# Performance work log

Hardware: AMD Instinct MI355X
Metric: run time of the kernel (lower is better)

Reference implementation:

```python
import jax, jax.numpy as jnp
import numpy as np

WS = 7        # window_size
SHIFT = 3     # shift_size
NH = 12       # num_heads
HD = 32       # head_dim
C = 384       # dim
HH = 56       # height
WW = 56       # width
EPS = 1e-5


def _rel_pos_index():
    coords = np.stack(np.meshgrid(np.arange(WS), np.arange(WS), indexing='ij')).reshape(2, -1)
    rel = (coords[:, :, None] - coords[:, None, :]).transpose(1, 2, 0)
    rel[:, :, 0] += WS - 1
    rel[:, :, 1] += WS - 1
    rel[:, :, 0] *= 2 * WS - 1
    return rel.sum(-1)  # (49, 49) int


def _attn_mask():
    # shift mask, computed statically (shift_size > 0 path)
    img = np.zeros((HH, WW))
    slices = (slice(0, -WS), slice(-WS, -SHIFT), slice(-SHIFT, None))
    cnt = 0
    for hs in slices:
        for ws in slices:
            img[hs, ws] = cnt
            cnt += 1
    mw = img.reshape(HH // WS, WS, WW // WS, WS).transpose(0, 2, 1, 3).reshape(-1, WS * WS)
    diff = mw[:, None, :] - mw[:, :, None]  # (nW, 49, 49)
    return np.where(diff != 0, -100.0, 0.0).astype(np.float32)


_REL_IDX = jnp.asarray(_rel_pos_index())
_MASK = jnp.asarray(_attn_mask())


def _layernorm(x, g, b):
    mu = jnp.mean(x, axis=-1, keepdims=True)
    var = jnp.mean(jnp.square(x - mu), axis=-1, keepdims=True)
    return (x - mu) * jax.lax.rsqrt(var + EPS) * g + b


def setup_inputs() -> dict:
    key = jax.random.key(0)
    ks = jax.random.split(key, 10)
    s = 0.02
    return {
        'hidden_states': jax.random.normal(ks[0], (32, HH * WW, C), jnp.float32),
        'ln1_g': jnp.ones((C,), jnp.float32),
        'ln1_b': jnp.zeros((C,), jnp.float32),
        'qkv_w': jax.random.normal(ks[1], (3 * C, C), jnp.float32) * s,
        'qkv_b': jnp.zeros((3 * C,), jnp.float32),
        'out_w': jax.random.normal(ks[2], (C, C), jnp.float32) * s,
        'out_b': jnp.zeros((C,), jnp.float32),
        'rel_bias_table': jax.random.normal(ks[3], ((2 * WS - 1) ** 2, NH), jnp.float32) * s,
        'ln2_g': jnp.ones((C,), jnp.float32),
        'ln2_b': jnp.zeros((C,), jnp.float32),
        'fc1_w': jax.random.normal(ks[4], (4 * C, C), jnp.float32) * s,
        'fc1_b': jnp.zeros((4 * C,), jnp.float32),
        'fc2_w': jax.random.normal(ks[5], (C, 4 * C), jnp.float32) * s,
        'fc2_b': jnp.zeros((C,), jnp.float32),
        'height': HH,
        'width': WW,
    }


def reference(hidden_states, ln1_g, ln1_b, qkv_w, qkv_b, out_w, out_b,
              rel_bias_table, ln2_g, ln2_b, fc1_w, fc1_b, fc2_w, fc2_b,
              height, width):
    B = hidden_states.shape[0]
    nWh, nWw = HH // WS, WW // WS
    nW = nWh * nWw
    L = WS * WS

    shortcut = hidden_states
    x = _layernorm(hidden_states, ln1_g, ln1_b).reshape(B, HH, WW, C)
    x = jnp.roll(x, (-SHIFT, -SHIFT), axis=(1, 2))
    # window partition -> (B*nW, 49, C)
    xw = x.reshape(B, nWh, WS, nWw, WS, C).transpose(0, 1, 3, 2, 4, 5).reshape(B * nW, L, C)

    qkv = xw @ qkv_w.T + qkv_b
    q, k, v = jnp.split(qkv, 3, axis=-1)
    q = q.reshape(-1, L, NH, HD).transpose(0, 2, 1, 3)  # (N, h, 49, d)
    k = k.reshape(-1, L, NH, HD).transpose(0, 2, 1, 3)
    v = v.reshape(-1, L, NH, HD).transpose(0, 2, 1, 3)

    scale = HD ** -0.5
    attn = jnp.einsum('nhqd,nhkd->nhqk', q, k) * scale
    bias = rel_bias_table[_REL_IDX.reshape(-1)].reshape(L, L, NH).transpose(2, 0, 1)  # (h, 49, 49)
    attn = attn + bias[None]
    attn = attn.reshape(B, nW, NH, L, L) + _MASK[None, :, None]
    attn = jax.nn.softmax(attn, axis=-1).reshape(B * nW, NH, L, L)

    out = jnp.einsum('nhqk,nhkd->nhqd', attn, v).transpose(0, 2, 1, 3).reshape(B * nW, L, C)
    out = out @ out_w.T + out_b

    # window reverse + un-shift
    out = out.reshape(B, nWh, nWw, WS, WS, C).transpose(0, 1, 3, 2, 4, 5).reshape(B, HH, WW, C)
    out = jnp.roll(out, (SHIFT, SHIFT), axis=(1, 2)).reshape(B, HH * WW, C)

    x = shortcut + out  # drop_path is identity (rate 0 / eval)
    h2 = _layernorm(x, ln2_g, ln2_b)
    mlp = jax.nn.gelu(h2 @ fc1_w.T + fc1_b, approximate=False) @ fc2_w.T + fc2_b
    return x + mlp
```

## Files before the change

### kernel.cpp

```cpp
#include <hip/hip_runtime.h>
#include <cstdint>
#include <cstddef>

using u16 = unsigned short;
using u32 = unsigned int;

typedef __attribute__((ext_vector_type(8))) short bf16x8;
typedef __attribute__((ext_vector_type(4))) float f32x4;

__device__ __forceinline__ u16 f2bf(float f) {
  union { float f; u32 u; } v; v.f = f;
  u32 r = v.u + 0x7FFFu + ((v.u >> 16) & 1u);
  return (u16)(r >> 16);
}
__device__ __forceinline__ float bf2f(u16 h) {
  union { u32 u; float f; } v; v.u = ((u32)h) << 16;
  return v.f;
}

__device__ __forceinline__ void gl_lds16(const void* g, void* l) {
  __builtin_amdgcn_global_load_lds(
      (const __attribute__((address_space(1))) void*)g,
      (__attribute__((address_space(3))) void*)l, 16, 0, 0);
}

__global__ __launch_bounds__(256) void k_f2bf(const float* __restrict__ s,
                                              u16* __restrict__ d, int n) {
  int i = blockIdx.x * 256 + threadIdx.x;
  if (i < n) d[i] = f2bf(s[i]);
}

__global__ __launch_bounds__(256) void k_tbl(const float* __restrict__ relt,
                                             float* __restrict__ tbl) {
  int id = blockIdx.x * 256 + threadIdx.x;
  if (id >= 196608) return;
  int i = id & 63, j = (id >> 6) & 63;
  int wt = (id >> 12) & 3, h = id >> 14;
  float v;
  if (j >= 49) {
    v = -3e38f;
  } else {
    int ii = i < 49 ? i : 48;
    int r1 = ii / 7, c1 = ii % 7, r2 = j / 7, c2 = j % 7;
    v = relt[((r1 - r2 + 6) * 13 + (c1 - c2 + 6)) * 12 + h];
    int rr1 = (wt & 2) ? (r1 < 4 ? 1 : 2) : 0;
    int rr2 = (wt & 2) ? (r2 < 4 ? 1 : 2) : 0;
    int cc1 = (wt & 1) ? (c1 < 4 ? 1 : 2) : 0;
    int cc2 = (wt & 1) ? (c2 < 4 ? 1 : 2) : 0;
    if (rr1 != rr2 || cc1 != cc2) v -= 100.f;
  }
  tbl[id] = v;
}

template <int GATHER>
__global__ __launch_bounds__(256) void k_ln(const float* __restrict__ x,
                                            const float* __restrict__ g,
                                            const float* __restrict__ b,
                                            u16* __restrict__ out) {
  int wave = threadIdx.x >> 6, lane = threadIdx.x & 63;
  int idx = blockIdx.x * 4 + wave;
  int src;
  if (GATHER) {
    int n = idx / 49, l = idx % 49;
    int bb = n >> 6, wi = n & 63;
    int wh = wi >> 3, ww = wi & 7;
    int r = l / 7, c = l % 7;
    int sr = wh * 7 + r + 3; if (sr >= 56) sr -= 56;
    int sc = ww * 7 + c + 3; if (sc >= 56) sc -= 56;
    src = bb * 3136 + sr * 56 + sc;
  } else {
    src = idx;
  }
  const float* xi = x + (size_t)src * 384;
  float2 v[3];
  float s = 0.f, sq = 0.f;
#pragma unroll
  for (int p = 0; p < 3; ++p) {
    v[p] = *(const float2*)(xi + p * 128 + lane * 2);
    s += v[p].x + v[p].y;
    sq += v[p].x * v[p].x + v[p].y * v[p].y;
  }
#pragma unroll
  for (int o = 32; o; o >>= 1) {
    s += __shfl_xor(s, o);
    sq += __shfl_xor(sq, o);
  }
  float mu = s * (1.f / 384.f);
  float var = sq * (1.f / 384.f) - mu * mu;
  float rstd = rsqrtf(var + 1e-5f);
  u16* oo = out + (size_t)idx * 384;
#pragma unroll
  for (int p = 0; p < 3; ++p) {
    int e = p * 128 + lane * 2;
    u16 o0 = f2bf((v[p].x - mu) * rstd * g[e] + b[e]);
    u16 o1 = f2bf((v[p].y - mu) * rstd * g[e + 1] + b[e + 1]);
    u32 pk = (u32)o0 | ((u32)o1 << 16);
    *(u32*)(oo + e) = pk;
  }
}

enum { EPI_QKV = 0, EPI_PROJ = 1, EPI_GELU = 2, EPI_FC2 = 3 };

template <int EPI>
__global__ __launch_bounds__(512, 2) void k_gemm3(
    const u16* __restrict__ A, const u16* __restrict__ Bw,
    const float* __restrict__ bias, u16* __restrict__ obf,
    float* __restrict__ of32, const float* __restrict__ addsrc,
    int K, int lda, int ldb, int ldc, int NT) {
  __shared__ u16 As[256 * 64];
  __shared__ u16 Bs[128 * 64];
  const int nwg = gridDim.x;
  const int q = nwg >> 3, r = nwg & 7;
  const int xcd = blockIdx.x & 7, rank = blockIdx.x >> 3;
  const int swz = (xcd < r ? xcd * (q + 1) : r * (q + 1) + (xcd - r) * q) + rank;
  const int m0 = (swz / NT) * 256, n0 = (swz % NT) * 128;

  const int tid = threadIdx.x;
  const int wid = tid >> 6, lane = tid & 63;
  const int wr = wid >> 1, wc = wid & 1;

  const int srow = tid >> 3;
  const int scol = 8 * ((tid & 7) ^ (srow & 7));
  const size_t abase = (size_t)(m0 + srow) * lda + scol;
  const size_t bbase = (size_t)(n0 + srow) * ldb + scol;
  const int dbase = wid * 512;

  f32x4 acc[4][4] = {};
  const int lrow = lane & 15;
  const int g8 = (lane >> 4) * 8;
  const int rx = (lrow & 7) << 3;

  const int NTK = K >> 6;

  for (int t = 0; t < NTK; ++t) {
    const int k0 = t << 6;
#pragma unroll
    for (int i = 0; i < 4; ++i)
      gl_lds16(A + abase + (size_t)(i * 64) * lda + k0,
               As + i * 4096 + dbase);
#pragma unroll
    for (int i = 0; i < 2; ++i)
      gl_lds16(Bw + bbase + (size_t)(i * 64) * ldb + k0,
               Bs + i * 4096 + dbase);
    __syncthreads();
    __builtin_amdgcn_s_setprio(1);
#pragma unroll
    for (int kk = 0; kk < 64; kk += 32) {
      bf16x8 af[4], bf[4];
#pragma unroll
      for (int mi = 0; mi < 4; ++mi) {
        int row = wr * 64 + mi * 16 + lrow;
        af[mi] = *(const bf16x8*)(&As[row * 64 + ((kk + g8) ^ rx)]);
      }
#pragma unroll
      for (int ni = 0; ni < 4; ++ni) {
        int row = wc * 64 + ni * 16 + lrow;
        bf[ni] = *(const bf16x8*)(&Bs[row * 64 + ((kk + g8) ^ rx)]);
      }
#pragma unroll
      for (int mi = 0; mi < 4; ++mi)
#pragma unroll
        for (int ni = 0; ni < 4; ++ni)
          acc[mi][ni] = __builtin_amdgcn_mfma_f32_16x16x32_bf16(
              af[mi], bf[ni], acc[mi][ni], 0, 0, 0);
    }
    __builtin_amdgcn_s_setprio(0);
    __syncthreads();
  }

  const int erow = (lane >> 4) * 4;
  const int ecol = lane & 15;
#pragma unroll
  for (int mi = 0; mi < 4; ++mi) {
#pragma unroll
    for (int ni = 0; ni < 4; ++ni) {
      int gcol = n0 + wc * 64 + ni * 16 + ecol;
      float bv = bias[gcol];
#pragma unroll
      for (int r4 = 0; r4 < 4; ++r4) {
        int grow = m0 + wr * 64 + mi * 16 + erow + r4;
        float v = acc[mi][ni][r4] + bv;
        if (EPI == EPI_QKV) {
          float vv = (gcol < 384) ? v * 0.17677669529663689f : v;
          obf[(size_t)grow * ldc + gcol] = f2bf(vv);
        } else if (EPI == EPI_GELU) {
          float gl = 0.5f * v * (1.f + erff(v * 0.70710678118f));
          obf[(size_t)grow * ldc + gcol] = f2bf(gl);
        } else if (EPI == EPI_PROJ) {
          int nwin = grow / 49, l = grow % 49;
          int bb = nwin >> 6, wi = nwin & 63;
          int wh = wi >> 3, ww = wi & 7;
          int rr = l / 7, cc = l % 7;
          int sr = wh * 7 + rr + 3; if (sr >= 56) sr -= 56;
          int sc = ww * 7 + cc + 3; if (sc >= 56) sc -= 56;
          size_t idx = ((size_t)(bb * 3136 + sr * 56 + sc)) * 384 + gcol;
          of32[idx] = addsrc[idx] + v;
        } else {
          size_t idx = (size_t)grow * 384 + gcol;
          of32[idx] = of32[idx] + v;
        }
      }
    }
  }
}

__global__ __launch_bounds__(64) void k_attn2(const u16* __restrict__ qkv,
                                              const float* __restrict__ tbl,
                                              u16* __restrict__ out) {
  __shared__ u16 P[64 * 64];
  const int bx = blockIdx.x;
  const int n = bx / 12, h = bx - n * 12;
  const int lane = threadIdx.x & 63;
  const int g = lane >> 4, c = lane & 15;
  const u16* base = qkv + (size_t)n * 56448 + h * 32;
  const int wi = n & 63;
  const int wt = (((wi >> 3) == 7) ? 2 : 0) | (((wi & 7) == 7) ? 1 : 0);
  const float* T = tbl + (size_t)((h << 2) | wt) * 4096;

  f32x4 st[4][4];
#pragma unroll
  for (int kj = 0; kj < 4; ++kj)
#pragma unroll
    for (int qi = 0; qi < 4; ++qi)
#pragma unroll
      for (int r = 0; r < 4; ++r)
        st[kj][qi][r] = T[(kj * 16 + g * 4 + r) * 64 + qi * 16 + c];

  bf16x8 qf[4], kf[4];
#pragma unroll
  for (int t = 0; t < 4; ++t) {
    int row = t * 16 + c; if (row > 48) row = 48;
    qf[t] = *(const bf16x8*)(base + (size_t)row * 1152 + g * 8);
    kf[t] = *(const bf16x8*)(base + (size_t)row * 1152 + 384 + g * 8);
  }

#pragma unroll
  for (int kj = 0; kj < 4; ++kj)
#pragma unroll
    for (int qi = 0; qi < 4; ++qi)
      st[kj][qi] = __builtin_amdgcn_mfma_f32_16x16x32_bf16(kf[kj], qf[qi],
                                                           st[kj][qi], 0, 0, 0);

#pragma unroll
  for (int qi = 0; qi < 4; ++qi) {
    float m = -3e38f;
#pragma unroll
    for (int kj = 0; kj < 4; ++kj)
#pragma unroll
      for (int r = 0; r < 4; ++r) m = fmaxf(m, st[kj][qi][r]);
    m = fmaxf(m, __shfl_xor(m, 16));
    m = fmaxf(m, __shfl_xor(m, 32));
    float sum = 0.f;
#pragma unroll
    for (int kj = 0; kj < 4; ++kj)
#pragma unroll
      for (int r = 0; r < 4; ++r) {
        float e = __expf(st[kj][qi][r] - m);
        st[kj][qi][r] = e;
        sum += e;
      }
    sum += __shfl_xor(sum, 16);
    sum += __shfl_xor(sum, 32);
    float inv = 1.f / sum;
    int i = qi * 16 + c;
#pragma unroll
    for (int kj = 0; kj < 4; ++kj)
#pragma unroll
      for (int hh = 0; hh < 2; ++hh) {
        u32 pk = (u32)f2bf(st[kj][qi][2 * hh] * inv) |
                 ((u32)f2bf(st[kj][qi][2 * hh + 1] * inv) << 16);
        int idx = (i * 64 + kj * 16 + g * 4 + 2 * hh) ^ ((i & 7) << 3);
        *(u32*)(P + idx) = pk;
      }
  }

  f32x4 o[4][2] = {};
#pragma unroll
  for (int k0 = 0; k0 < 2; ++k0) {
    bf16x8 pa[4], vb[2];
#pragma unroll
    for (int qi = 0; qi < 4; ++qi) {
      int qq = qi * 16 + c;
      pa[qi] = *(const bf16x8*)(P + ((qq * 64 + k0 * 32 + g * 8) ^ ((qq & 7) << 3)));
    }
#pragma unroll
    for (int ni = 0; ni < 2; ++ni) {
      union { bf16x8 v; u16 a[8]; } vu;
#pragma unroll
      for (int e = 0; e < 8; ++e) {
        int j = k0 * 32 + g * 8 + e;
        int jr = j > 48 ? 48 : j;
        vu.a[e] = base[(size_t)jr * 1152 + 768 + ni * 16 + c];
      }
      vb[ni] = vu.v;
#pragma unroll
      for (int qi = 0; qi < 4; ++qi)
        o[qi][ni] = __builtin_amdgcn_mfma_f32_16x16x32_bf16(pa[qi], vb[ni],
                                                            o[qi][ni], 0, 0, 0);
    }
  }

  u16* ob = out + (size_t)n * 18816 + h * 32;
#pragma unroll
  for (int qi = 0; qi < 4; ++qi)
#pragma unroll
    for (int r = 0; r < 4; ++r) {
      int qq = qi * 16 + g * 4 + r;
      if (qq < 49) {
#pragma unroll
        for (int ni = 0; ni < 2; ++ni)
          ob[(size_t)qq * 384 + ni * 16 + c] = f2bf(o[qi][ni][r]);
      }
    }
}

extern "C" void kernel_launch(void* const* d_in, const int* in_sizes, int n_in,
                              void* d_out, int out_size, void* d_ws,
                              size_t ws_size, hipStream_t stream) {
  const float* hidden = (const float*)d_in[0];
  const float* ln1g = (const float*)d_in[1];
  const float* ln1b = (const float*)d_in[2];
  const float* qkvw = (const float*)d_in[3];
  const float* qkvb = (const float*)d_in[4];
  const float* outw = (const float*)d_in[5];
  const float* outb = (const float*)d_in[6];
  const float* relt = (const float*)d_in[7];
  const float* ln2g = (const float*)d_in[8];
  const float* ln2b = (const float*)d_in[9];
  const float* fc1w = (const float*)d_in[10];
  const float* fc1b = (const float*)d_in[11];
  const float* fc2w = (const float*)d_in[12];
  const float* fc2b = (const float*)d_in[13];
  float* out = (float*)d_out;

  u16* wq = (u16*)d_ws;
  u16* wo = wq + 442368;
  u16* w1 = wo + 147456;
  u16* w2 = w1 + 589824;
  u16* xw = w2 + 589824;
  u16* qkv = xw + 38535168;
  u16* xn = qkv;
  u16* hbuf = xn + 38535168;
  float* tbl = (float*)wq;

  k_f2bf<<<1728, 256, 0, stream>>>(qkvw, wq, 442368);
  k_f2bf<<<576, 256, 0, stream>>>(outw, wo, 147456);
  k_f2bf<<<2304, 256, 0, stream>>>(fc1w, w1, 589824);
  k_f2bf<<<2304, 256, 0, stream>>>(fc2w, w2, 589824);

  k_ln<1><<<25088, 256, 0, stream>>>(hidden, ln1g, ln1b, xw);

  k_gemm3<EPI_QKV><<<392 * 9, 512, 0, stream>>>(
      xw, wq, qkvb, qkv, nullptr, nullptr, 384, 384, 384, 1152, 9);

  k_tbl<<<768, 256, 0, stream>>>(relt, tbl);

  k_attn2<<<24576, 64, 0, stream>>>(qkv, tbl, xw);

  k_gemm3<EPI_PROJ><<<392 * 3, 512, 0, stream>>>(
      xw, wo, outb, nullptr, out, hidden, 384, 384, 384, 384, 3);

  k_ln<0><<<25088, 256, 0, stream>>>(out, ln2g, ln2b, xn);

  for (int ch = 0; ch < 2; ++ch) {
    const u16* xa = xn + (size_t)ch * 50176 * 384;
    float* oc = out + (size_t)ch * 50176 * 384;
    k_gemm3<EPI_GELU><<<196 * 12, 512, 0, stream>>>(
        xa, w1, fc1b, hbuf, nullptr, nullptr, 384, 384, 384, 1536, 12);
    k_gemm3<EPI_FC2><<<196 * 3, 512, 0, stream>>>(
        hbuf, w2, fc2b, nullptr, oc, nullptr, 1536, 1536, 1536, 384, 3);
  }
}
```

Baseline: 891.6 us.

## Prefetch next K-tile in GEMM with double-buffered A and register-staged B

Measured after the change: 899.5 us. No clear change (+0.9%).

```diff
diff --git a/kernel.cpp b/kernel.cpp
--- a/kernel.cpp
+++ b/kernel.cpp
@@ -102,12 +102,12 @@
 enum { EPI_QKV = 0, EPI_PROJ = 1, EPI_GELU = 2, EPI_FC2 = 3 };
 
 template <int EPI>
-__global__ __launch_bounds__(512, 2) void k_gemm3(
+__global__ __launch_bounds__(512, 2) void k_gemm5(
     const u16* __restrict__ A, const u16* __restrict__ Bw,
     const float* __restrict__ bias, u16* __restrict__ obf,
     float* __restrict__ of32, const float* __restrict__ addsrc,
     int K, int lda, int ldb, int ldc, int NT) {
-  __shared__ u16 As[256 * 64];
+  __shared__ u16 As[2][256 * 64];
   __shared__ u16 Bs[128 * 64];
   const int nwg = gridDim.x;
   const int q = nwg >> 3, r = nwg & 7;
@@ -124,6 +124,7 @@
   const size_t abase = (size_t)(m0 + srow) * lda + scol;
   const size_t bbase = (size_t)(n0 + srow) * ldb + scol;
   const int dbase = wid * 512;
+  const int bwaddr = srow * 64 + (tid & 7) * 8;
 
   f32x4 acc[4][4] = {};
   const int lrow = lane & 15;
@@ -132,17 +133,30 @@
 
   const int NTK = K >> 6;
 
+  bf16x8 breg[2];
+#pragma unroll
+  for (int i = 0; i < 2; ++i)
+    breg[i] = *(const bf16x8*)(Bw + bbase + (size_t)(i * 64) * ldb);
+#pragma unroll
+  for (int i = 0; i < 4; ++i)
+    gl_lds16(A + abase + (size_t)(i * 64) * lda, As[0] + i * 4096 + dbase);
+#pragma unroll
+  for (int i = 0; i < 2; ++i)
+    *(bf16x8*)(&Bs[i * 4096 + bwaddr]) = breg[i];
+  __syncthreads();
+
   for (int t = 0; t < NTK; ++t) {
-    const int k0 = t << 6;
-#pragma unroll
-    for (int i = 0; i < 4; ++i)
-      gl_lds16(A + abase + (size_t)(i * 64) * lda + k0,
-               As + i * 4096 + dbase);
-#pragma unroll
-    for (int i = 0; i < 2; ++i)
-      gl_lds16(Bw + bbase + (size_t)(i * 64) * ldb + k0,
-               Bs + i * 4096 + dbase);
-    __syncthreads();
+    const int cur = t & 1;
+    if (t + 1 < NTK) {
+      const int k1 = (t + 1) << 6;
+#pragma unroll
+      for (int i = 0; i < 2; ++i)
+        breg[i] = *(const bf16x8*)(Bw + bbase + (size_t)(i * 64) * ldb + k1);
+#pragma unroll
+      for (int i = 0; i < 4; ++i)
+        gl_lds16(A + abase + (size_t)(i * 64) * lda + k1,
+                 As[cur ^ 1] + i * 4096 + dbase);
+    }
     __builtin_amdgcn_s_setprio(1);
 #pragma unroll
     for (int kk = 0; kk < 64; kk += 32) {
@@ -150,7 +164,7 @@
 #pragma unroll
       for (int mi = 0; mi < 4; ++mi) {
         int row = wr * 64 + mi * 16 + lrow;
-        af[mi] = *(const bf16x8*)(&As[row * 64 + ((kk + g8) ^ rx)]);
+        af[mi] = *(const bf16x8*)(&As[cur][row * 64 + ((kk + g8) ^ rx)]);
       }
 #pragma unroll
       for (int ni = 0; ni < 4; ++ni) {
@@ -165,6 +179,14 @@
               af[mi], bf[ni], acc[mi][ni], 0, 0, 0);
     }
     __builtin_amdgcn_s_setprio(0);
+    asm volatile("" ::: "memory");
+    __builtin_amdgcn_s_barrier();
+    asm volatile("" ::: "memory");
+    if (t + 1 < NTK) {
+#pragma unroll
+      for (int i = 0; i < 2; ++i)
+        *(bf16x8*)(&Bs[i * 4096 + bwaddr]) = breg[i];
+    }
     __syncthreads();
   }
 
@@ -350,14 +372,14 @@
 
   k_ln<1><<<25088, 256, 0, stream>>>(hidden, ln1g, ln1b, xw);
 
-  k_gemm3<EPI_QKV><<<392 * 9, 512, 0, stream>>>(
+  k_gemm5<EPI_QKV><<<392 * 9, 512, 0, stream>>>(
       xw, wq, qkvb, qkv, nullptr, nullptr, 384, 384, 384, 1152, 9);
 
   k_tbl<<<768, 256, 0, stream>>>(relt, tbl);
 
   k_attn2<<<24576, 64, 0, stream>>>(qkv, tbl, xw);
 
-  k_gemm3<EPI_PROJ><<<392 * 3, 512, 0, stream>>>(
+  k_gemm5<EPI_PROJ><<<392 * 3, 512, 0, stream>>>(
       xw, wo, outb, nullptr, out, hidden, 384, 384, 384, 384, 3);
 
   k_ln<0><<<25088, 256, 0, stream>>>(out, ln2g, ln2b, xn);
@@ -365,9 +387,9 @@
   for (int ch = 0; ch < 2; ++ch) {
     const u16* xa = xn + (size_t)ch * 50176 * 384;
     float* oc = out + (size_t)ch * 50176 * 384;
-    k_gemm3<EPI_GELU><<<196 * 12, 512, 0, stream>>>(
+    k_gemm5<EPI_GELU><<<196 * 12, 512, 0, stream>>>(
         xa, w1, fc1b, hbuf, nullptr, nullptr, 384, 384, 384, 1536, 12);
-    k_gemm3<EPI_FC2><<<196 * 3, 512, 0, stream>>>(
+    k_gemm5<EPI_FC2><<<196 * 3, 512, 0, stream>>>(
         hbuf, w2, fc2b, nullptr, oc, nullptr, 1536, 1536, 1536, 384, 3);
   }
 }
```

## Emit transposed V from QKV GEMM and vectorize V loads in attention

Applied to the files above, without the earlier changes.

Result: slower. 954.4 us (+7.1%).

```diff
diff --git a/kernel.cpp b/kernel.cpp
--- a/kernel.cpp
+++ b/kernel.cpp
@@ -24,10 +24,16 @@
       (__attribute__((address_space(3))) void*)l, 16, 0, 0);
 }
 
-__global__ __launch_bounds__(256) void k_f2bf(const float* __restrict__ s,
-                                              u16* __restrict__ d, int n) {
+__global__ __launch_bounds__(256) void k_f2bf4(
+    const float* __restrict__ a0, const float* __restrict__ a1,
+    const float* __restrict__ a2, const float* __restrict__ a3,
+    u16* __restrict__ d0, u16* __restrict__ d1, u16* __restrict__ d2,
+    u16* __restrict__ d3) {
   int i = blockIdx.x * 256 + threadIdx.x;
-  if (i < n) d[i] = f2bf(s[i]);
+  if (i < 442368) d0[i] = f2bf(a0[i]);
+  else if (i < 589824) d1[i - 442368] = f2bf(a1[i - 442368]);
+  else if (i < 1179648) d2[i - 589824] = f2bf(a2[i - 589824]);
+  else if (i < 1769472) d3[i - 1179648] = f2bf(a3[i - 1179648]);
 }
 
 __global__ __launch_bounds__(256) void k_tbl(const float* __restrict__ relt,
@@ -106,7 +112,7 @@
     const u16* __restrict__ A, const u16* __restrict__ Bw,
     const float* __restrict__ bias, u16* __restrict__ obf,
     float* __restrict__ of32, const float* __restrict__ addsrc,
-    int K, int lda, int ldb, int ldc, int NT) {
+    u16* __restrict__ vtout, int K, int lda, int ldb, int ldc, int NT) {
   __shared__ u16 As[256 * 64];
   __shared__ u16 Bs[128 * 64];
   const int nwg = gridDim.x;
@@ -181,8 +187,13 @@
         int grow = m0 + wr * 64 + mi * 16 + erow + r4;
         float v = acc[mi][ni][r4] + bv;
         if (EPI == EPI_QKV) {
-          float vv = (gcol < 384) ? v * 0.17677669529663689f : v;
-          obf[(size_t)grow * ldc + gcol] = f2bf(vv);
+          if (gcol < 768) {
+            float vv = (gcol < 384) ? v * 0.17677669529663689f : v;
+            obf[(size_t)grow * ldc + gcol] = f2bf(vv);
+          } else {
+            int nwin = grow / 49, l = grow - nwin * 49;
+            vtout[((size_t)nwin * 384 + (gcol - 768)) * 64 + l] = f2bf(v);
+          }
         } else if (EPI == EPI_GELU) {
           float gl = 0.5f * v * (1.f + erff(v * 0.70710678118f));
           obf[(size_t)grow * ldc + gcol] = f2bf(gl);
@@ -204,7 +215,8 @@
   }
 }
 
-__global__ __launch_bounds__(64) void k_attn2(const u16* __restrict__ qkv,
+__global__ __launch_bounds__(64) void k_attn3(const u16* __restrict__ qk,
+                                              const u16* __restrict__ vt,
                                               const float* __restrict__ tbl,
                                               u16* __restrict__ out) {
   __shared__ u16 P[64 * 64];
@@ -212,7 +224,7 @@
   const int n = bx / 12, h = bx - n * 12;
   const int lane = threadIdx.x & 63;
   const int g = lane >> 4, c = lane & 15;
-  const u16* base = qkv + (size_t)n * 56448 + h * 32;
+  const u16* base = qk + (size_t)n * 49 * 768 + h * 32;
   const int wi = n & 63;
   const int wt = (((wi >> 3) == 7) ? 2 : 0) | (((wi & 7) == 7) ? 1 : 0);
   const float* T = tbl + (size_t)((h << 2) | wt) * 4096;
@@ -230,8 +242,8 @@
 #pragma unroll
   for (int t = 0; t < 4; ++t) {
     int row = t * 16 + c; if (row > 48) row = 48;
-    qf[t] = *(const bf16x8*)(base + (size_t)row * 1152 + g * 8);
-    kf[t] = *(const bf16x8*)(base + (size_t)row * 1152 + 384 + g * 8);
+    qf[t] = *(const bf16x8*)(base + (size_t)row * 768 + g * 8);
+    kf[t] = *(const bf16x8*)(base + (size_t)row * 768 + 384 + g * 8);
   }
 
 #pragma unroll
@@ -274,6 +286,7 @@
       }
   }
 
+  const u16* vbase = vt + ((size_t)n * 384 + h * 32) * 64;
   f32x4 o[4][2] = {};
 #pragma unroll
   for (int k0 = 0; k0 < 2; ++k0) {
@@ -284,20 +297,15 @@
       pa[qi] = *(const bf16x8*)(P + ((qq * 64 + k0 * 32 + g * 8) ^ ((qq & 7) << 3)));
     }
 #pragma unroll
-    for (int ni = 0; ni < 2; ++ni) {
-      union { bf16x8 v; u16 a[8]; } vu;
-#pragma unroll
-      for (int e = 0; e < 8; ++e) {
-        int j = k0 * 32 + g * 8 + e;
-        int jr = j > 48 ? 48 : j;
-        vu.a[e] = base[(size_t)jr * 1152 + 768 + ni * 16 + c];
-      }
-      vb[ni] = vu.v;
+    for (int ni = 0; ni < 2; ++ni)
+      vb[ni] = *(const bf16x8*)(vbase + (size_t)(ni * 16 + c) * 64 + k0 * 32 +
+                                g * 8);
+#pragma unroll
+    for (int ni = 0; ni < 2; ++ni)
 #pragma unroll
       for (int qi = 0; qi < 4; ++qi)
         o[qi][ni] = __builtin_amdgcn_mfma_f32_16x16x32_bf16(pa[qi], vb[ni],
                                                             o[qi][ni], 0, 0, 0);
-    }
   }
 
   u16* ob = out + (size_t)n * 18816 + h * 32;
@@ -338,27 +346,25 @@
   u16* w1 = wo + 147456;
   u16* w2 = w1 + 589824;
   u16* xw = w2 + 589824;
-  u16* qkv = xw + 38535168;
-  u16* xn = qkv;
-  u16* hbuf = xn + 38535168;
+  u16* qk = xw + 38535168;
+  u16* vT = qk + 77070336;
+  u16* xn = qk;
+  u16* hbuf = qk + 38535168;
   float* tbl = (float*)wq;
 
-  k_f2bf<<<1728, 256, 0, stream>>>(qkvw, wq, 442368);
-  k_f2bf<<<576, 256, 0, stream>>>(outw, wo, 147456);
-  k_f2bf<<<2304, 256, 0, stream>>>(fc1w, w1, 589824);
-  k_f2bf<<<2304, 256, 0, stream>>>(fc2w, w2, 589824);
+  k_f2bf4<<<6912, 256, 0, stream>>>(qkvw, outw, fc1w, fc2w, wq, wo, w1, w2);
 
   k_ln<1><<<25088, 256, 0, stream>>>(hidden, ln1g, ln1b, xw);
 
   k_gemm3<EPI_QKV><<<392 * 9, 512, 0, stream>>>(
-      xw, wq, qkvb, qkv, nullptr, nullptr, 384, 384, 384, 1152, 9);
+      xw, wq, qkvb, qk, nullptr, nullptr, vT, 384, 384, 384, 768, 9);
 
   k_tbl<<<768, 256, 0, stream>>>(relt, tbl);
 
-  k_attn2<<<24576, 64, 0, stream>>>(qkv, tbl, xw);
+  k_attn3<<<24576, 64, 0, stream>>>(qk, vT, tbl, xw);
 
   k_gemm3<EPI_PROJ><<<392 * 3, 512, 0, stream>>>(
-      xw, wo, outb, nullptr, out, hidden, 384, 384, 384, 384, 3);
+      xw, wo, outb, nullptr, out, hidden, nullptr, 384, 384, 384, 384, 3);
 
   k_ln<0><<<25088, 256, 0, stream>>>(out, ln2g, ln2b, xn);
 
@@ -366,8 +372,8 @@
     const u16* xa = xn + (size_t)ch * 50176 * 384;
     float* oc = out + (size_t)ch * 50176 * 384;
     k_gemm3<EPI_GELU><<<196 * 12, 512, 0, stream>>>(
-        xa, w1, fc1b, hbuf, nullptr, nullptr, 384, 384, 384, 1536, 12);
+        xa, w1, fc1b, hbuf, nullptr, nullptr, nullptr, 384, 384, 384, 1536, 12);
     k_gemm3<EPI_FC2><<<196 * 3, 512, 0, stream>>>(
-        hbuf, w2, fc2b, nullptr, oc, nullptr, 1536, 1536, 1536, 384, 3);
-  }
-}
+        hbuf, w2, fc2b, nullptr, oc, nullptr, nullptr, 1536, 1536, 1536, 384, 3);
+  }
+}
```
